# Performance work log

Hardware: AMD Instinct MI355X
Metric: run time of the kernel (lower is better)

The kernel has to match this reference:

```python
import jax, jax.numpy as jnp
import numpy as np

N_NODES = 100000
N_EDGES = 3200000
IN_FEATS = 256
OUT_FEATS = 128
N_LAYERS = 3


def setup_inputs() -> dict:
    key = jax.random.key(0)
    k1, k2, k3, k4, k5, k6 = jax.random.split(key, 6)
    x = jax.random.normal(k1, (N_NODES, IN_FEATS), dtype=jnp.float32)
    row = jax.random.randint(k2, (N_EDGES,), 0, N_NODES, dtype=jnp.int64)
    col = jax.random.randint(k3, (N_EDGES,), 0, N_NODES, dtype=jnp.int64)
    vals = jax.random.uniform(k4, (N_EDGES,), dtype=jnp.float32)
    W = jax.random.normal(k5, (OUT_FEATS, IN_FEATS), dtype=jnp.float32) * (1.0 / np.sqrt(IN_FEATS))
    b = jax.random.normal(k6, (OUT_FEATS,), dtype=jnp.float32) * 0.01
    return {"x": x, "row": row, "col": col, "vals": vals, "W": W, "b": b, "n_layers": N_LAYERS}


def reference(x, row, col, vals, W, b, n_layers):
    n_nodes = x.shape[0]
    # z = linear(x)
    z = jnp.einsum('ni,oi->no', x, W) + b  # [N, out_feats]
    # repeated SpMM: z_new[r] = sum over edges e with row[e]==r of vals[e] * z[col[e]]
    for _ in range(int(n_layers)):
        gathered = vals[:, None] * z[col]  # [E, out_feats]
        z = jax.ops.segment_sum(gathered, row, num_segments=n_nodes)
    return z
```

## Files before the change

kernel.cpp:

```cpp
#include <hip/hip_runtime.h>
#include <hip/hip_bf16.h>

#define NNODES   100000
#define INF      256
#define OUTF     128
#define NLAYERS  3

#define RPB   196
#define NBKT  511
#define CAP   7168
#define EPB   4096

typedef unsigned short u16;

__device__ __forceinline__ float bf2f(u16 u) {
    union { unsigned int i; float f; } c; c.i = ((unsigned int)u) << 16; return c.f;
}
__device__ __forceinline__ u16 f2bf(float f) {
    union { float f; unsigned int i; } c; c.f = f;
    unsigned int lsb = (c.i >> 16) & 1;
    return (u16)((c.i + 0x7FFF + lsb) >> 16);
}

__global__ __launch_bounds__(256) void partition_kernel(
    const int* __restrict__ row, const int* __restrict__ col,
    const float* __restrict__ vals, int* __restrict__ alloc,
    int2* __restrict__ epart, int E)
{
    __shared__ int srow[EPB];
    __shared__ int hist[NBKT];
    __shared__ int gbase[NBKT];
    int tid = threadIdx.x;
    int e0  = blockIdx.x * EPB;

    for (int i = tid; i < NBKT; i += 256) hist[i] = 0;
    __syncthreads();
    for (int i = tid; i < EPB; i += 256) {
        int e = e0 + i;
        int r = (e < E) ? row[e] : -1;
        srow[i] = r;
        if (r >= 0) atomicAdd(&hist[r / RPB], 1);
    }
    __syncthreads();
    for (int i = tid; i < NBKT; i += 256) {
        int c = hist[i];
        gbase[i] = c ? atomicAdd(&alloc[i], c) : 0;
    }
    __syncthreads();
    for (int i = tid; i < NBKT; i += 256) hist[i] = 0;
    __syncthreads();
    for (int i = tid; i < EPB; i += 256) {
        int r = srow[i];
        if (r >= 0) {
            int b    = r / RPB;
            int lofs = atomicAdd(&hist[b], 1);
            int pos  = gbase[b] + lofs;
            int e    = e0 + i;
            epart[(size_t)b * CAP + pos] =
                make_int2(col[e] | ((r - b * RPB) << 17), __float_as_int(vals[e]));
        }
    }
}

__global__ __launch_bounds__(256) void bucket_scatter_kernel(
    const int* __restrict__ alloc, int2* __restrict__ epart,
    int* __restrict__ rowptr, int* __restrict__ rowcnt, int M)
{
    int b = blockIdx.x;
    int n = alloc[b];
    int2* src = epart + (size_t)b * CAP;
    __shared__ int2 stage[CAP];
    __shared__ int  hist[256];
    __shared__ int  excl[256];
    __shared__ int  wofs[RPB];
    int tid = threadIdx.x;

    for (int i = tid; i < n; i += 256) stage[i] = src[i];
    hist[tid] = 0;
    __syncthreads();
    for (int i = tid; i < n; i += 256) atomicAdd(&hist[stage[i].x >> 17], 1);
    __syncthreads();
    int v = hist[tid];
    excl[tid] = v;
    __syncthreads();
    for (int off = 1; off < 256; off <<= 1) {
        int t = (tid >= off) ? excl[tid - off] : 0;
        __syncthreads();
        excl[tid] += t;
        __syncthreads();
    }
    int ex = excl[tid] - v;
    int r  = b * RPB + tid;
    if (tid < RPB && r < M) {
        rowptr[r] = b * CAP + ex;
        rowcnt[r] = v;
    }
    if (tid < RPB) wofs[tid] = ex;
    __syncthreads();
    for (int i = tid; i < n; i += 256) {
        int2 p  = stage[i];
        int  rl = p.x >> 17;
        int  pos = atomicAdd(&wofs[rl], 1);
        src[pos] = make_int2(p.x & 0x1FFFF, p.y);
    }
}

__global__ __launch_bounds__(256) void gemm_kernel(const float* __restrict__ x,
                                                   const float* __restrict__ W,
                                                   const float* __restrict__ b,
                                                   u16* __restrict__ z, int M) {
    __shared__ float xs[32][65];
    __shared__ float Ws[128][65];
    int tid = threadIdx.x;
    int n0  = blockIdx.x * 32;
    int oi  = tid & 31;
    int ni  = (tid >> 5) * 4;

    float bo[4];
#pragma unroll
    for (int j = 0; j < 4; ++j) bo[j] = b[oi + 32 * j];
    float acc[4][4];
#pragma unroll
    for (int i = 0; i < 4; ++i)
#pragma unroll
        for (int j = 0; j < 4; ++j) acc[i][j] = bo[j];

    for (int k0 = 0; k0 < INF; k0 += 64) {
        {
            int rrow = tid >> 3, kk = (tid & 7) * 8;
            int nn = n0 + rrow; if (nn >= M) nn = M - 1;
            const float* src = x + (size_t)nn * INF + k0 + kk;
            float4 a0 = ((const float4*)src)[0];
            float4 a1 = ((const float4*)src)[1];
            xs[rrow][kk + 0] = a0.x; xs[rrow][kk + 1] = a0.y;
            xs[rrow][kk + 2] = a0.z; xs[rrow][kk + 3] = a0.w;
            xs[rrow][kk + 4] = a1.x; xs[rrow][kk + 5] = a1.y;
            xs[rrow][kk + 6] = a1.z; xs[rrow][kk + 7] = a1.w;
        }
        {
            int rrow = tid >> 1, kk = (tid & 1) * 32;
            const float* src = W + (size_t)rrow * INF + k0 + kk;
#pragma unroll
            for (int t = 0; t < 8; ++t) {
                float4 a = ((const float4*)src)[t];
                Ws[rrow][kk + 4 * t + 0] = a.x; Ws[rrow][kk + 4 * t + 1] = a.y;
                Ws[rrow][kk + 4 * t + 2] = a.z; Ws[rrow][kk + 4 * t + 3] = a.w;
            }
        }
        __syncthreads();
#pragma unroll 4
        for (int k = 0; k < 64; ++k) {
            float xv[4], wv[4];
#pragma unroll
            for (int i = 0; i < 4; ++i) xv[i] = xs[ni + i][k];
#pragma unroll
            for (int j = 0; j < 4; ++j) wv[j] = Ws[oi + 32 * j][k];
#pragma unroll
            for (int i = 0; i < 4; ++i)
#pragma unroll
                for (int j = 0; j < 4; ++j) acc[i][j] += xv[i] * wv[j];
        }
        __syncthreads();
    }
#pragma unroll
    for (int i = 0; i < 4; ++i) {
        int nn = n0 + ni + i;
        if (nn < M) {
#pragma unroll
            for (int j = 0; j < 4; ++j)
                z[(size_t)nn * OUTF + oi + 32 * j] = f2bf(acc[i][j]);
        }
    }
}

template <bool MASKED>
__device__ __forceinline__ void edge8(const int2* __restrict__ ep, int e, int end,
                                      const u16* __restrict__ zin, int f,
                                      float2* __restrict__ acc) {
    int2 p[8];
#pragma unroll
    for (int i = 0; i < 8; ++i) {
        int idx = MASKED ? ((e + i < end) ? e + i : end - 1) : (e + i);
        p[i] = ep[idx];
    }
    ushort2 zb[8];
#pragma unroll
    for (int i = 0; i < 8; ++i)
        zb[i] = *(const ushort2*)(zin + (size_t)p[i].x * OUTF + f);
#pragma unroll
    for (int i = 0; i < 8; ++i) {
        float v = __int_as_float(p[i].y);
        if (MASKED) v = (e + i < end) ? v : 0.f;
        acc[i & 3].x += v * bf2f(zb[i].x);
        acc[i & 3].y += v * bf2f(zb[i].y);
    }
}

template <bool OUT_BF16>
__global__ __launch_bounds__(256) void spmm_kernel(const int* __restrict__ rowptr,
                                                   const int* __restrict__ rowcnt,
                                                   const int2* __restrict__ epart,
                                                   const u16* __restrict__ zin,
                                                   void* __restrict__ zout, int M) {
    int r = blockIdx.x * 4 + (threadIdx.x >> 6);
    if (r >= M) return;
    int lane = threadIdx.x & 63;
    int f    = lane * 2;

    int start = __builtin_amdgcn_readfirstlane(rowptr[r]);
    int n     = __builtin_amdgcn_readfirstlane(rowcnt[r]);
    int end   = start + n;

    float2 acc[4] = {{0.f,0.f},{0.f,0.f},{0.f,0.f},{0.f,0.f}};
    int e = start;
    for (; e + 8 <= end; e += 8) edge8<false>(epart, e, end, zin, f, acc);
    if (e < end)                 edge8<true >(epart, e, end, zin, f, acc);

    float sx = (acc[0].x + acc[1].x) + (acc[2].x + acc[3].x);
    float sy = (acc[0].y + acc[1].y) + (acc[2].y + acc[3].y);
    if (OUT_BF16) {
        ushort2 o; o.x = f2bf(sx); o.y = f2bf(sy);
        *(ushort2*)((u16*)zout + (size_t)r * OUTF + f) = o;
    } else {
        *(float2*)((float*)zout + (size_t)r * OUTF + f) = make_float2(sx, sy);
    }
}


extern "C" void kernel_launch(void* const* d_in, const int* in_sizes, int n_in,
                              void* d_out, int out_size, void* d_ws, size_t ws_size,
                              hipStream_t stream) {
    const float* x    = (const float*)d_in[0];
    const int*   row  = (const int*)d_in[1];
    const int*   col  = (const int*)d_in[2];
    const float* vals = (const float*)d_in[3];
    const float* W    = (const float*)d_in[4];
    const float* b    = (const float*)d_in[5];
    float* out = (float*)d_out;

    const int M = in_sizes[0] / INF;
    const int E = in_sizes[1];

    u16*   zb0    = (u16*)d_ws;
    u16*   zb1    = zb0 + (size_t)M * OUTF;
    int*   rowptr = (int*)(zb1 + (size_t)M * OUTF);
    int*   rowcnt = rowptr + M;
    int*   alloc  = rowcnt + M;
    size_t ofs = (size_t)((char*)(alloc + NBKT) - (char*)d_ws);
    ofs = (ofs + 7) & ~(size_t)7;
    int2*  epart  = (int2*)((char*)d_ws + ofs);

    hipMemsetAsync(alloc, 0, NBKT * sizeof(int), stream);
    partition_kernel<<<(E + EPB - 1) / EPB, 256, 0, stream>>>(row, col, vals, alloc, epart, E);
    bucket_scatter_kernel<<<NBKT, 256, 0, stream>>>(alloc, epart, rowptr, rowcnt, M);

    gemm_kernel<<<(M + 31) / 32, 256, 0, stream>>>(x, W, b, zb0, M);

    int sgrid = (M + 3) / 4;
    spmm_kernel<true ><<<sgrid, 256, 0, stream>>>(rowptr, rowcnt, epart, zb0, (void*)zb1, M);
    spmm_kernel<true ><<<sgrid, 256, 0, stream>>>(rowptr, rowcnt, epart, zb1, (void*)zb0, M);
    spmm_kernel<false><<<sgrid, 256, 0, stream>>>(rowptr, rowcnt, epart, zb0, (void*)out, M);
}
```

Measured before the change: 706.0 us.

## Replace FP32 SIMT linear layer with bf16 MFMA GEMM

Rewrites the dense linear projection as a matrix-core kernel using 16x16x32 bf16 MFMA instructions. Each block stages all of W in shared memory as bf16 with an XOR swizzle to avoid bank conflicts. Each wave computes 16 rows and converts x to bf16 in registers. This cuts the FP32 FMA cost of the GEMM, but the input is now rounded to bf16, which adds precision error. The block also needs 64KB of LDS, which may limit occupancy.

```diff
diff --git a/kernel.cpp b/kernel.cpp
--- a/kernel.cpp
+++ b/kernel.cpp
@@ -12,6 +12,9 @@
 #define EPB   4096
 
 typedef unsigned short u16;
+
+typedef __attribute__((ext_vector_type(8))) __bf16 bf16x8;
+typedef __attribute__((ext_vector_type(4))) float  f32x4;
 
 __device__ __forceinline__ float bf2f(u16 u) {
     union { unsigned int i; float f; } c; c.i = ((unsigned int)u) << 16; return c.f;
@@ -105,70 +108,78 @@
     }
 }
 
-__global__ __launch_bounds__(256) void gemm_kernel(const float* __restrict__ x,
-                                                   const float* __restrict__ W,
-                                                   const float* __restrict__ b,
-                                                   u16* __restrict__ z, int M) {
-    __shared__ float xs[32][65];
-    __shared__ float Ws[128][65];
-    int tid = threadIdx.x;
-    int n0  = blockIdx.x * 32;
-    int oi  = tid & 31;
-    int ni  = (tid >> 5) * 4;
-
-    float bo[4];
-#pragma unroll
-    for (int j = 0; j < 4; ++j) bo[j] = b[oi + 32 * j];
-    float acc[4][4];
-#pragma unroll
-    for (int i = 0; i < 4; ++i)
-#pragma unroll
-        for (int j = 0; j < 4; ++j) acc[i][j] = bo[j];
-
-    for (int k0 = 0; k0 < INF; k0 += 64) {
-        {
-            int rrow = tid >> 3, kk = (tid & 7) * 8;
-            int nn = n0 + rrow; if (nn >= M) nn = M - 1;
-            const float* src = x + (size_t)nn * INF + k0 + kk;
-            float4 a0 = ((const float4*)src)[0];
-            float4 a1 = ((const float4*)src)[1];
-            xs[rrow][kk + 0] = a0.x; xs[rrow][kk + 1] = a0.y;
-            xs[rrow][kk + 2] = a0.z; xs[rrow][kk + 3] = a0.w;
-            xs[rrow][kk + 4] = a1.x; xs[rrow][kk + 5] = a1.y;
-            xs[rrow][kk + 6] = a1.z; xs[rrow][kk + 7] = a1.w;
-        }
-        {
-            int rrow = tid >> 1, kk = (tid & 1) * 32;
-            const float* src = W + (size_t)rrow * INF + k0 + kk;
-#pragma unroll
-            for (int t = 0; t < 8; ++t) {
-                float4 a = ((const float4*)src)[t];
-                Ws[rrow][kk + 4 * t + 0] = a.x; Ws[rrow][kk + 4 * t + 1] = a.y;
-                Ws[rrow][kk + 4 * t + 2] = a.z; Ws[rrow][kk + 4 * t + 3] = a.w;
-            }
-        }
-        __syncthreads();
-#pragma unroll 4
-        for (int k = 0; k < 64; ++k) {
-            float xv[4], wv[4];
-#pragma unroll
-            for (int i = 0; i < 4; ++i) xv[i] = xs[ni + i][k];
-#pragma unroll
-            for (int j = 0; j < 4; ++j) wv[j] = Ws[oi + 32 * j][k];
-#pragma unroll
-            for (int i = 0; i < 4; ++i)
-#pragma unroll
-                for (int j = 0; j < 4; ++j) acc[i][j] += xv[i] * wv[j];
-        }
-        __syncthreads();
-    }
-#pragma unroll
-    for (int i = 0; i < 4; ++i) {
-        int nn = n0 + ni + i;
-        if (nn < M) {
-#pragma unroll
-            for (int j = 0; j < 4; ++j)
-                z[(size_t)nn * OUTF + oi + 32 * j] = f2bf(acc[i][j]);
+__global__ __launch_bounds__(256) void gemm_mfma_kernel(
+    const float* __restrict__ x, const float* __restrict__ W,
+    const float* __restrict__ b, u16* __restrict__ z, int M)
+{
+    __shared__ __align__(16) u16 Wl[128 * 256];
+    int tid  = threadIdx.x;
+    int lane = tid & 63;
+    int wv   = tid >> 6;
+
+    {
+        int c  = tid >> 1;
+        int k0 = (tid & 1) * 128;
+        const float* src = W + (size_t)c * INF + k0;
+        u16* dst = Wl + c * 256;
+        int swz = (c & 7) << 3;
+#pragma unroll
+        for (int t = 0; t < 32; ++t) {
+            float4 a = ((const float4*)src)[t];
+            int k = (k0 + 4 * t) ^ swz;
+            dst[k + 0] = f2bf(a.x); dst[k + 1] = f2bf(a.y);
+            dst[k + 2] = f2bf(a.z); dst[k + 3] = f2bf(a.w);
+        }
+    }
+
+    int cl = lane & 15;
+    int g  = lane >> 4;
+    float bo[8];
+#pragma unroll
+    for (int f = 0; f < 8; ++f) bo[f] = b[16 * f + cl];
+
+    __syncthreads();
+
+    int n0 = blockIdx.x * 64 + wv * 16;
+    int nr = n0 + cl;
+    if (nr >= M) nr = M - 1;
+    const float* xrow = x + (size_t)nr * INF + 8 * g;
+
+    f32x4 acc[8];
+#pragma unroll
+    for (int f = 0; f < 8; ++f) {
+        f32x4 a; a[0] = bo[f]; a[1] = bo[f]; a[2] = bo[f]; a[3] = bo[f];
+        acc[f] = a;
+    }
+
+#pragma unroll
+    for (int ks = 0; ks < 8; ++ks) {
+        int k0 = ks * 32;
+        float4 a0 = ((const float4*)(xrow + k0))[0];
+        float4 a1 = ((const float4*)(xrow + k0))[1];
+        bf16x8 af;
+        af[0] = (__bf16)a0.x; af[1] = (__bf16)a0.y;
+        af[2] = (__bf16)a0.z; af[3] = (__bf16)a0.w;
+        af[4] = (__bf16)a1.x; af[5] = (__bf16)a1.y;
+        af[6] = (__bf16)a1.z; af[7] = (__bf16)a1.w;
+#pragma unroll
+        for (int f = 0; f < 8; ++f) {
+            int c  = 16 * f + cl;
+            int ke = (k0 + 8 * g) ^ ((c & 7) << 3);
+            bf16x8 bfr = *(const bf16x8*)(Wl + c * 256 + ke);
+            acc[f] = __builtin_amdgcn_mfma_f32_16x16x32_bf16(af, bfr, acc[f], 0, 0, 0);
+        }
+    }
+
+    int rbase = n0 + 4 * g;
+#pragma unroll
+    for (int j = 0; j < 4; ++j) {
+        int n = rbase + j;
+        if (n < M) {
+            u16* zr = z + (size_t)n * OUTF;
+#pragma unroll
+            for (int f = 0; f < 8; ++f)
+                zr[16 * f + cl] = f2bf(acc[f][j]);
         }
     }
 }
@@ -254,7 +265,7 @@
     partition_kernel<<<(E + EPB - 1) / EPB, 256, 0, stream>>>(row, col, vals, alloc, epart, E);
     bucket_scatter_kernel<<<NBKT, 256, 0, stream>>>(alloc, epart, rowptr, rowcnt, M);
 
-    gemm_kernel<<<(M + 31) / 32, 256, 0, stream>>>(x, W, b, zb0, M);
+    gemm_mfma_kernel<<<(M + 63) / 64, 256, 0, stream>>>(x, W, b, zb0, M);
 
     int sgrid = (M + 3) / 4;
     spmm_kernel<true ><<<sgrid, 256, 0, stream>>>(rowptr, rowcnt, epart, zb0, (void*)zb1, M);
```

Result: faster. 646.2 us (-8.5%).
